# Kernel tuning notes

Hardware: AMD Instinct MI355X
Metric: run time of the kernel (lower is better)

Reference implementation:

```python
import jax, jax.numpy as jnp
import numpy as np
import math

ANSWER_LEN = 11
D_MODEL = 6
MAX_SEQ_LEN = 34
POS_DIM = 3
TOK_DIM = 3
HEAD_DIM = 3
N_HEADS = 2
FFN_DIM = 6
VOCAB_SIZE = 14
B = 65536
T = 34
EPS = 1e-5


def setup_inputs() -> dict:
    key = jax.random.key(0)
    ks = jax.random.split(key, 16)
    s = 0.1
    return {
        "idx": jax.random.randint(ks[0], (B, T), 0, VOCAB_SIZE, dtype=jnp.int32),
        "tok_emb": jax.random.normal(ks[1], (VOCAB_SIZE, TOK_DIM), jnp.float32) * s,
        "pos_enc": jax.random.normal(ks[2], (MAX_SEQ_LEN, POS_DIM), jnp.float32) * s,
        "wq": jax.random.normal(ks[3], (POS_DIM, N_HEADS * HEAD_DIM), jnp.float32) * s,
        "wk": jax.random.normal(ks[4], (POS_DIM, N_HEADS * HEAD_DIM), jnp.float32) * s,
        "wv": jax.random.normal(ks[5], (TOK_DIM, N_HEADS * HEAD_DIM), jnp.float32) * s,
        "wo": jax.random.normal(ks[6], (N_HEADS * HEAD_DIM, D_MODEL), jnp.float32) * s,
        "ln1_g": jnp.ones((D_MODEL,), jnp.float32),
        "ln1_b": jnp.zeros((D_MODEL,), jnp.float32),
        "ln2_g": jnp.ones((D_MODEL,), jnp.float32),
        "ln2_b": jnp.zeros((D_MODEL,), jnp.float32),
        "w1": jax.random.normal(ks[7], (D_MODEL, FFN_DIM), jnp.float32) * s,
        "b1": jnp.zeros((FFN_DIM,), jnp.float32),
        "w2": jax.random.normal(ks[8], (FFN_DIM, D_MODEL), jnp.float32) * s,
        "b2": jnp.zeros((D_MODEL,), jnp.float32),
        "lnf_g": jnp.ones((D_MODEL,), jnp.float32),
        "lnf_b": jnp.zeros((D_MODEL,), jnp.float32),
        "w_head": jax.random.normal(ks[9], (D_MODEL, VOCAB_SIZE), jnp.float32) * s,
    }


def _layernorm(x, g, b):
    mu = jnp.mean(x, axis=-1, keepdims=True)
    var = jnp.var(x, axis=-1, keepdims=True)
    return (x - mu) * jax.lax.rsqrt(var + EPS) * g + b


def _attn(x, wq, wk, wv, wo):
    Bt, Tt, _ = x.shape
    x_tok = x[:, :, :TOK_DIM]   # [B,T,3]
    x_pos = x[:, :, TOK_DIM:]   # [B,T,3]
    q = (x_pos @ wq).reshape(Bt, Tt, N_HEADS, HEAD_DIM)
    k = (x_pos @ wk).reshape(Bt, Tt, N_HEADS, HEAD_DIM)
    v = (x_tok @ wv).reshape(Bt, Tt, N_HEADS, HEAD_DIM)
    scores = jnp.einsum('bqhd,bkhd->bhqk', q, k) / math.sqrt(HEAD_DIM)
    causal = jnp.tril(jnp.ones((Tt, Tt), bool))
    scores = jnp.where(causal, scores, -jnp.inf)
    attn = jax.nn.softmax(scores, axis=-1)
    out = jnp.einsum('bhqk,bkhd->bqhd', attn, v).reshape(Bt, Tt, N_HEADS * HEAD_DIM)
    return out @ wo


def reference(idx, tok_emb, pos_enc, wq, wk, wv, wo, ln1_g, ln1_b, ln2_g, ln2_b,
              w1, b1, w2, b2, lnf_g, lnf_b, w_head):
    Bt, Tt = idx.shape
    tok = tok_emb[idx]                                   # [B,T,3]
    pos = jnp.broadcast_to(pos_enc[:Tt][None], (Bt, Tt, POS_DIM))
    x = jnp.concatenate([tok, pos], axis=-1)             # [B,T,6]
    x = x + _attn(_layernorm(x, ln1_g, ln1_b), wq, wk, wv, wo)
    h = _layernorm(x, ln2_g, ln2_b)
    x = x + (jax.nn.gelu(h @ w1 + b1, approximate=False) @ w2 + b2)
    x = _layernorm(x, lnf_g, lnf_b)
    return x @ w_head                                    # [B,T,VOCAB]
```

## Files before the change

kernel.cpp:

```cpp
#include <hip/hip_runtime.h>
#include <math.h>

#define T_SEQ 34
#define VOCAB 14
#define NE (T_SEQ * VOCAB)
#define SEQS 64
#define BLK 576
#define NBLK 1024
#define OFFP 35

__device__ __forceinline__ void layernorm6(const float* x, const float* g,
                                           const float* bt, float* o) {
    float mu = (x[0] + x[1] + x[2] + x[3] + x[4] + x[5]) * (1.0f / 6.0f);
    float var = 0.0f;
#pragma unroll
    for (int i = 0; i < 6; ++i) { float d = x[i] - mu; var += d * d; }
    var *= (1.0f / 6.0f);
    float rs = rsqrtf(var + 1e-5f);
#pragma unroll
    for (int i = 0; i < 6; ++i) o[i] = (x[i] - mu) * rs * g[i] + bt[i];
}

template <int NT>
__device__ __forceinline__ void run_rows(
    int T0, int seq, int blk,
    const float4* __restrict__ kvA, const float4* __restrict__ kvB,
    const float4* __restrict__ kvC,
    const float4* __restrict__ qA,  const float2* __restrict__ qB,
    const float4* __restrict__ xA,  const float2* __restrict__ xB,
    const int* __restrict__ myoff,
    const float* __restrict__ wo,
    const float* __restrict__ ln2_g, const float* __restrict__ ln2_b,
    const float* __restrict__ w1,   const float* __restrict__ b1,
    const float* __restrict__ w2,   const float* __restrict__ b2,
    const float* __restrict__ lnf_g, const float* __restrict__ lnf_b,
    const float* __restrict__ w_head,
    float* __restrict__ out)
{
    float q[NT][6];
#pragma unroll
    for (int i = 0; i < NT; ++i) {
        const int e = myoff[T0 + i];
        const float4 a = qA[e]; const float2 b2v = qB[e];
        q[i][0] = a.x; q[i][1] = a.y; q[i][2] = a.z;
        q[i][3] = a.w; q[i][4] = b2v.x; q[i][5] = b2v.y;
    }
    float den0[NT], den1[NT], acc[NT][6];
#pragma unroll
    for (int i = 0; i < NT; ++i) {
        den0[i] = 0.f; den1[i] = 0.f;
#pragma unroll
        for (int j = 0; j < 6; ++j) acc[i][j] = 0.f;
    }

    auto body = [&](int e, int imin) {
        const float4 ea = kvA[e], eb = kvB[e], ec = kvC[e];
#pragma unroll
        for (int i = 0; i < NT; ++i) {
            if (i >= imin) {
                const float s0 = q[i][0] * ea.x + q[i][1] * ea.y + q[i][2] * ea.z;
                const float s1 = q[i][3] * ea.w + q[i][4] * eb.x + q[i][5] * eb.y;
                const float p0 = exp2f(s0);
                const float p1 = exp2f(s1);
                den0[i] += p0; den1[i] += p1;
                acc[i][0] += p0 * eb.z; acc[i][1] += p0 * eb.w; acc[i][2] += p0 * ec.x;
                acc[i][3] += p1 * ec.y; acc[i][4] += p1 * ec.z; acc[i][5] += p1 * ec.w;
            }
        }
    };

    for (int s = 0; s < T0; ++s) body(myoff[s], 0);
#pragma unroll
    for (int j = 0; j < NT; ++j) body(myoff[T0 + j], j);

#pragma unroll
    for (int i = 0; i < NT; ++i) {
        const int t = T0 + i;
        const int e = myoff[t];
        const float inv0 = __builtin_amdgcn_rcpf(den0[i]);
        const float inv1 = __builtin_amdgcn_rcpf(den1[i]);
        float ao[6];
#pragma unroll
        for (int d = 0; d < 3; ++d) { ao[d] = acc[i][d] * inv0; ao[3 + d] = acc[i][3 + d] * inv1; }
        const float4 xa = xA[e]; const float2 xb = xB[e];
        const float x[6] = {xa.x, xa.y, xa.z, xa.w, xb.x, xb.y};
        float x2[6];
#pragma unroll
        for (int j = 0; j < 6; ++j) {
            float s = x[j];
#pragma unroll
            for (int k = 0; k < 6; ++k) s += ao[k] * wo[k * 6 + j];
            x2[j] = s;
        }
        float h[6];
        layernorm6(x2, ln2_g, ln2_b, h);
        float f[6];
#pragma unroll
        for (int j = 0; j < 6; ++j) {
            float s = b1[j];
#pragma unroll
            for (int k = 0; k < 6; ++k) s += h[k] * w1[k * 6 + j];
            f[j] = 0.5f * s * (1.0f + erff(s * 0.70710678118654752f));
        }
        float x3[6];
#pragma unroll
        for (int j = 0; j < 6; ++j) {
            float s = x2[j] + b2[j];
#pragma unroll
            for (int k = 0; k < 6; ++k) s += f[k] * w2[k * 6 + j];
            x3[j] = s;
        }
        float xo[6];
        layernorm6(x3, lnf_g, lnf_b, xo);

        const size_t g = ((size_t)(blk * SEQS + seq)) * T_SEQ + t;
        float2* op = (float2*)(out + g * 14);
#pragma unroll
        for (int jj = 0; jj < 7; ++jj) {
            float o0 = 0.f, o1 = 0.f;
#pragma unroll
            for (int k = 0; k < 6; ++k) {
                o0 += xo[k] * w_head[k * 14 + 2 * jj];
                o1 += xo[k] * w_head[k * 14 + 2 * jj + 1];
            }
            op[jj] = make_float2(o0, o1);
        }
    }
}

__global__ __launch_bounds__(BLK, 5) void fused_tf_kernel(
    const int* __restrict__ idx,
    const float* __restrict__ tok_emb,
    const float* __restrict__ pos_enc,
    const float* __restrict__ wq,
    const float* __restrict__ wk,
    const float* __restrict__ wv,
    const float* __restrict__ wo,
    const float* __restrict__ ln1_g, const float* __restrict__ ln1_b,
    const float* __restrict__ ln2_g, const float* __restrict__ ln2_b,
    const float* __restrict__ w1,   const float* __restrict__ b1,
    const float* __restrict__ w2,   const float* __restrict__ b2,
    const float* __restrict__ lnf_g, const float* __restrict__ lnf_b,
    const float* __restrict__ w_head,
    float* __restrict__ out)
{
    __shared__ float4 kvA[NE];
    __shared__ float4 kvB[NE];
    __shared__ float4 kvC[NE];
    __shared__ float4 qA[NE];
    __shared__ float2 qB[NE];
    __shared__ float4 xA[NE];
    __shared__ float2 xB[NE];
    __shared__ int offt[SEQS * OFFP];

    const int tid = threadIdx.x;

    for (int i = tid; i < SEQS * T_SEQ; i += BLK) {
        const int sq = i / T_SEQ;
        const int s  = i - sq * T_SEQ;
        const int tok = idx[(size_t)blockIdx.x * (SEQS * T_SEQ) + i];
        offt[sq * OFFP + s] = s * VOCAB + tok;
    }

    if (tid < NE) {
        const int t = tid / VOCAB;
        const int v = tid - t * VOCAB;
        float x[6];
#pragma unroll
        for (int i = 0; i < 3; ++i) x[i] = tok_emb[v * 3 + i];
#pragma unroll
        for (int i = 0; i < 3; ++i) x[3 + i] = pos_enc[t * 3 + i];
        float xl[6];
        layernorm6(x, ln1_g, ln1_b, xl);
        const float kscale = 0.8329812666744317f;
        float qv[6], kv6[6], vv[6];
#pragma unroll
        for (int j = 0; j < 6; ++j) {
            qv[j]  =  xl[3] * wq[j] + xl[4] * wq[6 + j] + xl[5] * wq[12 + j];
            kv6[j] = (xl[3] * wk[j] + xl[4] * wk[6 + j] + xl[5] * wk[12 + j]) * kscale;
            vv[j]  =  xl[0] * wv[j] + xl[1] * wv[6 + j] + xl[2] * wv[12 + j];
        }
        kvA[tid] = make_float4(kv6[0], kv6[1], kv6[2], kv6[3]);
        kvB[tid] = make_float4(kv6[4], kv6[5], vv[0], vv[1]);
        kvC[tid] = make_float4(vv[2], vv[3], vv[4], vv[5]);
        qA[tid]  = make_float4(qv[0], qv[1], qv[2], qv[3]);
        qB[tid]  = make_float2(qv[4], qv[5]);
        xA[tid]  = make_float4(x[0], x[1], x[2], x[3]);
        xB[tid]  = make_float2(x[4], x[5]);
    }
    __syncthreads();

    const int seq = tid & 63;
    const int grp = tid >> 6;
    const int* myoff = &offt[seq * OFFP];

    if (grp < 8)
        run_rows<4>(4 * grp, seq, blockIdx.x, kvA, kvB, kvC, qA, qB, xA, xB,
                    myoff, wo, ln2_g, ln2_b, w1, b1, w2, b2, lnf_g, lnf_b,
                    w_head, out);
    else
        run_rows<2>(32, seq, blockIdx.x, kvA, kvB, kvC, qA, qB, xA, xB,
                    myoff, wo, ln2_g, ln2_b, w1, b1, w2, b2, lnf_g, lnf_b,
                    w_head, out);
}

extern "C" void kernel_launch(void* const* d_in, const int* in_sizes, int n_in,
                              void* d_out, int out_size, void* d_ws, size_t ws_size,
                              hipStream_t stream) {
    const int*   idx     = (const int*)d_in[0];
    const float* tok_emb = (const float*)d_in[1];
    const float* pos_enc = (const float*)d_in[2];
    const float* wq      = (const float*)d_in[3];
    const float* wk      = (const float*)d_in[4];
    const float* wv      = (const float*)d_in[5];
    const float* wo      = (const float*)d_in[6];
    const float* ln1_g   = (const float*)d_in[7];
    const float* ln1_b   = (const float*)d_in[8];
    const float* ln2_g   = (const float*)d_in[9];
    const float* ln2_b   = (const float*)d_in[10];
    const float* w1      = (const float*)d_in[11];
    const float* b1      = (const float*)d_in[12];
    const float* w2      = (const float*)d_in[13];
    const float* b2      = (const float*)d_in[14];
    const float* lnf_g   = (const float*)d_in[15];
    const float* lnf_b   = (const float*)d_in[16];
    const float* w_head  = (const float*)d_in[17];
    float* out = (float*)d_out;

    hipLaunchKernelGGL(fused_tf_kernel, dim3(NBLK), dim3(BLK), 0, stream,
                       idx, tok_emb, pos_enc, wq, wk, wv, wo,
                       ln1_g, ln1_b, ln2_g, ln2_b, w1, b1, w2, b2,
                       lnf_g, lnf_b, w_head, out);
}
```

Baseline: 277.3 us.

## Stage output logits through shared memory for coalesced global stores

Each thread's logits are now written into an LDS staging buffer that reuses the attention tables' space, one half of the block's sequences at a time. The whole block then copies that buffer to global memory with contiguous, coalesced float2 stores, replacing the per-thread strided 56-byte row writes. The change also rebuilds the residual input from small token and position tables instead of per-entry xA/xB arrays, and switches exp2f with a log2e-folded scale to __expf with a plain 1/sqrt(3) scale. In exchange it adds block barriers and an extra LDS round trip, and the last group redundantly recomputes rows 30–31.

```diff
diff --git a/kernel.cpp b/kernel.cpp
--- a/kernel.cpp
+++ b/kernel.cpp
@@ -3,11 +3,12 @@
 
 #define T_SEQ 34
 #define VOCAB 14
-#define NE (T_SEQ * VOCAB)
+#define NE 476
 #define SEQS 64
 #define BLK 576
 #define NBLK 1024
 #define OFFP 35
+#define LDS_BYTES 61184
 
 __device__ __forceinline__ void layernorm6(const float* x, const float* g,
                                            const float* bt, float* o) {
@@ -19,113 +20,6 @@
     float rs = rsqrtf(var + 1e-5f);
 #pragma unroll
     for (int i = 0; i < 6; ++i) o[i] = (x[i] - mu) * rs * g[i] + bt[i];
-}
-
-template <int NT>
-__device__ __forceinline__ void run_rows(
-    int T0, int seq, int blk,
-    const float4* __restrict__ kvA, const float4* __restrict__ kvB,
-    const float4* __restrict__ kvC,
-    const float4* __restrict__ qA,  const float2* __restrict__ qB,
-    const float4* __restrict__ xA,  const float2* __restrict__ xB,
-    const int* __restrict__ myoff,
-    const float* __restrict__ wo,
-    const float* __restrict__ ln2_g, const float* __restrict__ ln2_b,
-    const float* __restrict__ w1,   const float* __restrict__ b1,
-    const float* __restrict__ w2,   const float* __restrict__ b2,
-    const float* __restrict__ lnf_g, const float* __restrict__ lnf_b,
-    const float* __restrict__ w_head,
-    float* __restrict__ out)
-{
-    float q[NT][6];
-#pragma unroll
-    for (int i = 0; i < NT; ++i) {
-        const int e = myoff[T0 + i];
-        const float4 a = qA[e]; const float2 b2v = qB[e];
-        q[i][0] = a.x; q[i][1] = a.y; q[i][2] = a.z;
-        q[i][3] = a.w; q[i][4] = b2v.x; q[i][5] = b2v.y;
-    }
-    float den0[NT], den1[NT], acc[NT][6];
-#pragma unroll
-    for (int i = 0; i < NT; ++i) {
-        den0[i] = 0.f; den1[i] = 0.f;
-#pragma unroll
-        for (int j = 0; j < 6; ++j) acc[i][j] = 0.f;
-    }
-
-    auto body = [&](int e, int imin) {
-        const float4 ea = kvA[e], eb = kvB[e], ec = kvC[e];
-#pragma unroll
-        for (int i = 0; i < NT; ++i) {
-            if (i >= imin) {
-                const float s0 = q[i][0] * ea.x + q[i][1] * ea.y + q[i][2] * ea.z;
-                const float s1 = q[i][3] * ea.w + q[i][4] * eb.x + q[i][5] * eb.y;
-                const float p0 = exp2f(s0);
-                const float p1 = exp2f(s1);
-                den0[i] += p0; den1[i] += p1;
-                acc[i][0] += p0 * eb.z; acc[i][1] += p0 * eb.w; acc[i][2] += p0 * ec.x;
-                acc[i][3] += p1 * ec.y; acc[i][4] += p1 * ec.z; acc[i][5] += p1 * ec.w;
-            }
-        }
-    };
-
-    for (int s = 0; s < T0; ++s) body(myoff[s], 0);
-#pragma unroll
-    for (int j = 0; j < NT; ++j) body(myoff[T0 + j], j);
-
-#pragma unroll
-    for (int i = 0; i < NT; ++i) {
-        const int t = T0 + i;
-        const int e = myoff[t];
-        const float inv0 = __builtin_amdgcn_rcpf(den0[i]);
-        const float inv1 = __builtin_amdgcn_rcpf(den1[i]);
-        float ao[6];
-#pragma unroll
-        for (int d = 0; d < 3; ++d) { ao[d] = acc[i][d] * inv0; ao[3 + d] = acc[i][3 + d] * inv1; }
-        const float4 xa = xA[e]; const float2 xb = xB[e];
-        const float x[6] = {xa.x, xa.y, xa.z, xa.w, xb.x, xb.y};
-        float x2[6];
-#pragma unroll
-        for (int j = 0; j < 6; ++j) {
-            float s = x[j];
-#pragma unroll
-            for (int k = 0; k < 6; ++k) s += ao[k] * wo[k * 6 + j];
-            x2[j] = s;
-        }
-        float h[6];
-        layernorm6(x2, ln2_g, ln2_b, h);
-        float f[6];
-#pragma unroll
-        for (int j = 0; j < 6; ++j) {
-            float s = b1[j];
-#pragma unroll
-            for (int k = 0; k < 6; ++k) s += h[k] * w1[k * 6 + j];
-            f[j] = 0.5f * s * (1.0f + erff(s * 0.70710678118654752f));
-        }
-        float x3[6];
-#pragma unroll
-        for (int j = 0; j < 6; ++j) {
-            float s = x2[j] + b2[j];
-#pragma unroll
-            for (int k = 0; k < 6; ++k) s += f[k] * w2[k * 6 + j];
-            x3[j] = s;
-        }
-        float xo[6];
-        layernorm6(x3, lnf_g, lnf_b, xo);
-
-        const size_t g = ((size_t)(blk * SEQS + seq)) * T_SEQ + t;
-        float2* op = (float2*)(out + g * 14);
-#pragma unroll
-        for (int jj = 0; jj < 7; ++jj) {
-            float o0 = 0.f, o1 = 0.f;
-#pragma unroll
-            for (int k = 0; k < 6; ++k) {
-                o0 += xo[k] * w_head[k * 14 + 2 * jj];
-                o1 += xo[k] * w_head[k * 14 + 2 * jj + 1];
-            }
-            op[jj] = make_float2(o0, o1);
-        }
-    }
 }
 
 __global__ __launch_bounds__(BLK, 5) void fused_tf_kernel(
@@ -144,23 +38,27 @@
     const float* __restrict__ w_head,
     float* __restrict__ out)
 {
-    __shared__ float4 kvA[NE];
-    __shared__ float4 kvB[NE];
-    __shared__ float4 kvC[NE];
-    __shared__ float4 qA[NE];
-    __shared__ float2 qB[NE];
-    __shared__ float4 xA[NE];
-    __shared__ float2 xB[NE];
-    __shared__ int offt[SEQS * OFFP];
+    extern __shared__ __align__(16) unsigned char uS[];
+    float4* kvA  = (float4*)(uS + 0);
+    float4* kvB  = (float4*)(uS + 7616);
+    float4* kvC  = (float4*)(uS + 15232);
+    float4* qA   = (float4*)(uS + 22848);
+    float2* qB   = (float2*)(uS + 30464);
+    int*    offt = (int*)  (uS + 34272);
+    float2* o2   = (float2*)uS;
+
+    __shared__ float temb[VOCAB * 3];
+    __shared__ float penc[T_SEQ * 3];
 
     const int tid = threadIdx.x;
 
     for (int i = tid; i < SEQS * T_SEQ; i += BLK) {
         const int sq = i / T_SEQ;
         const int s  = i - sq * T_SEQ;
-        const int tok = idx[(size_t)blockIdx.x * (SEQS * T_SEQ) + i];
-        offt[sq * OFFP + s] = s * VOCAB + tok;
-    }
+        offt[sq * OFFP + s] = s * VOCAB + idx[(size_t)blockIdx.x * (SEQS * T_SEQ) + i];
+    }
+    if (tid < VOCAB * 3) temb[tid] = tok_emb[tid];
+    if (tid < T_SEQ * 3) penc[tid] = pos_enc[tid];
 
     if (tid < NE) {
         const int t = tid / VOCAB;
@@ -172,7 +70,7 @@
         for (int i = 0; i < 3; ++i) x[3 + i] = pos_enc[t * 3 + i];
         float xl[6];
         layernorm6(x, ln1_g, ln1_b, xl);
-        const float kscale = 0.8329812666744317f;
+        const float kscale = 0.57735026918962576f;
         float qv[6], kv6[6], vv[6];
 #pragma unroll
         for (int j = 0; j < 6; ++j) {
@@ -185,23 +83,120 @@
         kvC[tid] = make_float4(vv[2], vv[3], vv[4], vv[5]);
         qA[tid]  = make_float4(qv[0], qv[1], qv[2], qv[3]);
         qB[tid]  = make_float2(qv[4], qv[5]);
-        xA[tid]  = make_float4(x[0], x[1], x[2], x[3]);
-        xB[tid]  = make_float2(x[4], x[5]);
     }
     __syncthreads();
 
     const int seq = tid & 63;
     const int grp = tid >> 6;
+    const int T0  = (grp == 8) ? 30 : (grp << 2);
     const int* myoff = &offt[seq * OFFP];
 
-    if (grp < 8)
-        run_rows<4>(4 * grp, seq, blockIdx.x, kvA, kvB, kvC, qA, qB, xA, xB,
-                    myoff, wo, ln2_g, ln2_b, w1, b1, w2, b2, lnf_g, lnf_b,
-                    w_head, out);
-    else
-        run_rows<2>(32, seq, blockIdx.x, kvA, kvB, kvC, qA, qB, xA, xB,
-                    myoff, wo, ln2_g, ln2_b, w1, b1, w2, b2, lnf_g, lnf_b,
-                    w_head, out);
+    float q[4][6]; int tokR[4];
+#pragma unroll
+    for (int i = 0; i < 4; ++i) {
+        const int e = myoff[T0 + i];
+        tokR[i] = e - VOCAB * (T0 + i);
+        const float4 a = qA[e]; const float2 bb = qB[e];
+        q[i][0] = a.x; q[i][1] = a.y; q[i][2] = a.z;
+        q[i][3] = a.w; q[i][4] = bb.x; q[i][5] = bb.y;
+    }
+    float den0[4], den1[4], acc[4][6];
+#pragma unroll
+    for (int i = 0; i < 4; ++i) {
+        den0[i] = 0.f; den1[i] = 0.f;
+#pragma unroll
+        for (int j = 0; j < 6; ++j) acc[i][j] = 0.f;
+    }
+
+    auto body = [&](int e, int imin) {
+        const float4 ea = kvA[e]; const float4 eb = kvB[e]; const float4 ec = kvC[e];
+#pragma unroll
+        for (int i = 0; i < 4; ++i) {
+            if (i >= imin) {
+                const float s0 = q[i][0] * ea.x + q[i][1] * ea.y + q[i][2] * ea.z;
+                const float s1 = q[i][3] * ea.w + q[i][4] * eb.x + q[i][5] * eb.y;
+                const float p0 = __expf(s0);
+                const float p1 = __expf(s1);
+                den0[i] += p0; den1[i] += p1;
+                acc[i][0] += p0 * eb.z; acc[i][1] += p0 * eb.w; acc[i][2] += p0 * ec.x;
+                acc[i][3] += p1 * ec.y; acc[i][4] += p1 * ec.z; acc[i][5] += p1 * ec.w;
+            }
+        }
+    };
+    for (int s = 0; s < T0; ++s) body(myoff[s], 0);
+#pragma unroll
+    for (int j = 0; j < 4; ++j) body(myoff[T0 + j], j);
+
+    for (int c = 0; c < 2; ++c) {
+        __syncthreads();
+        if ((seq >> 5) == c) {
+            const int sL = seq & 31;
+#pragma unroll
+            for (int i = 0; i < 4; ++i) {
+                const int t = T0 + i;
+                const float inv0 = __builtin_amdgcn_rcpf(den0[i]);
+                const float inv1 = __builtin_amdgcn_rcpf(den1[i]);
+                float ao[6];
+#pragma unroll
+                for (int d = 0; d < 3; ++d) {
+                    ao[d]     = acc[i][d]     * inv0;
+                    ao[3 + d] = acc[i][3 + d] * inv1;
+                }
+                float x[6];
+#pragma unroll
+                for (int k = 0; k < 3; ++k) {
+                    x[k]     = temb[tokR[i] * 3 + k];
+                    x[3 + k] = penc[t * 3 + k];
+                }
+                float x2[6];
+#pragma unroll
+                for (int j = 0; j < 6; ++j) {
+                    float s = x[j];
+#pragma unroll
+                    for (int k = 0; k < 6; ++k) s += ao[k] * wo[k * 6 + j];
+                    x2[j] = s;
+                }
+                float h[6];
+                layernorm6(x2, ln2_g, ln2_b, h);
+                float f[6];
+#pragma unroll
+                for (int j = 0; j < 6; ++j) {
+                    float s = b1[j];
+#pragma unroll
+                    for (int k = 0; k < 6; ++k) s += h[k] * w1[k * 6 + j];
+                    f[j] = 0.5f * s * (1.0f + erff(s * 0.70710678118654752f));
+                }
+                float x3[6];
+#pragma unroll
+                for (int j = 0; j < 6; ++j) {
+                    float s = x2[j] + b2[j];
+#pragma unroll
+                    for (int k = 0; k < 6; ++k) s += f[k] * w2[k * 6 + j];
+                    x3[j] = s;
+                }
+                float xo[6];
+                layernorm6(x3, lnf_g, lnf_b, xo);
+
+                float2* orow = &o2[sL * 239 + t * 7];
+#pragma unroll
+                for (int jj = 0; jj < 7; ++jj) {
+                    float o0 = 0.f, o1 = 0.f;
+#pragma unroll
+                    for (int k = 0; k < 6; ++k) {
+                        o0 += xo[k] * w_head[k * 14 + 2 * jj];
+                        o1 += xo[k] * w_head[k * 14 + 2 * jj + 1];
+                    }
+                    orow[jj] = make_float2(o0, o1);
+                }
+            }
+        }
+        __syncthreads();
+        float2* dst = (float2*)(out + ((size_t)blockIdx.x * SEQS + c * 32) * (T_SEQ * 14));
+        for (int i = tid; i < 32 * T_SEQ * 7; i += BLK) {
+            const unsigned sq = (unsigned)i / 238u;
+            dst[i] = o2[i + sq];
+        }
+    }
 }
 
 extern "C" void kernel_launch(void* const* d_in, const int* in_sizes, int n_in,
@@ -227,7 +222,7 @@
     const float* w_head  = (const float*)d_in[17];
     float* out = (float*)d_out;
 
-    hipLaunchKernelGGL(fused_tf_kernel, dim3(NBLK), dim3(BLK), 0, stream,
+    hipLaunchKernelGGL(fused_tf_kernel, dim3(NBLK), dim3(BLK), LDS_BYTES, stream,
                        idx, tok_emb, pos_enc, wq, wk, wv, wo,
                        ln1_g, ln1_b, ln2_g, ln2_b, w1, b1, w2, b2,
                        lnf_g, lnf_b, w_head, out);
```

Result: slower. 288.6 us (+4.1%).
